# Kernel optimization log

Measured on AMD Instinct MI355X. Metric: run time of the kernel, lower is better.

## Reference

```python
import jax, jax.numpy as jnp
import numpy as np

D_MODEL = 1024
EPS_DT = 1e-4
LN_EPS = 1e-5


def _layernorm(y, gamma, beta):
    mu = jnp.mean(y, axis=-1, keepdims=True)
    var = jnp.var(y, axis=-1, keepdims=True)
    return (y - mu) * jax.lax.rsqrt(var + LN_EPS) * gamma + beta


def setup_inputs() -> dict:
    key = jax.random.key(0)
    ks = jax.random.split(key, 8)
    B, T, D = 8, 4096, D_MODEL
    s = 1.0 / np.sqrt(D)  # ~ torch Linear default init scale
    return {
        "x": jax.random.normal(ks[0], (B, T, D), jnp.float32),
        "delta_t": jax.random.uniform(ks[1], (B, T, D), jnp.float32),
        "log_decay": jnp.zeros((D,), jnp.float32),
        "W_in": jax.random.uniform(ks[2], (D, D), jnp.float32, -s, s),
        "b_in": jax.random.uniform(ks[3], (D,), jnp.float32, -s, s),
        "W_gate": jax.random.uniform(ks[4], (D, D), jnp.float32, -s, s),
        "b_gate": jax.random.uniform(ks[5], (D,), jnp.float32, -s, s),
        "W_out": jax.random.uniform(ks[6], (D, D), jnp.float32, -s, s),
        "b_out": jax.random.uniform(ks[7], (D,), jnp.float32, -s, s),
        "gamma": jnp.ones((D,), jnp.float32),
        "beta": jnp.zeros((D,), jnp.float32),
    }


def reference(x, delta_t, log_decay, W_in, b_in, W_gate, b_gate, W_out, b_out, gamma, beta):
    B, T, D = x.shape
    decay = jax.nn.softplus(log_decay) + 1e-4          # [D]
    dt = jnp.maximum(delta_t, EPS_DT)                   # [B,T,D]
    lamb = jnp.exp(-decay * dt)                         # [B,T,D]
    # Drive terms depend only on x -> precompute in parallel (big GEMMs).
    update = jnp.einsum('btd,ed->bte', x, W_in) + b_in
    gate = jax.nn.sigmoid(jnp.einsum('btd,ed->bte', x, W_gate) + b_gate)
    drive = (1.0 - lamb) * gate * update                # [B,T,D]

    def step(state, inputs):
        l_t, d_t = inputs
        state = l_t * state + d_t
        return state, state

    state0 = jnp.zeros((B, D), x.dtype)
    final_state, states = jax.lax.scan(
        step, state0,
        (jnp.swapaxes(lamb, 0, 1), jnp.swapaxes(drive, 0, 1)))
    states = jnp.swapaxes(states, 0, 1)                 # [B,T,D]
    # dropout is identity in eval mode
    y = states + jnp.einsum('btd,ed->bte', states, W_out) + b_out
    out = _layernorm(y, gamma, beta)
    return out, final_state
```

## Files before the change

### kernel.cpp

```cpp
#include <hip/hip_runtime.h>
#include <hip/hip_bf16.h>

#define D_MODEL 1024
#define BATCH 8
#define SEQ 4096
#define MROWS (BATCH*SEQ)
#define NC 64
#define CL 64

typedef __attribute__((ext_vector_type(4))) float f32x4;
typedef __attribute__((ext_vector_type(8))) short s16x8;

__device__ __forceinline__ unsigned short f2bf(float f){
  union { float f; unsigned int u; } v; v.f = f;
  return (unsigned short)((v.u + 0x7fffu + ((v.u >> 16) & 1u)) >> 16);
}
__device__ __forceinline__ float bf2f(unsigned int bits){
  union { unsigned int u; float f; } v; v.u = bits << 16; return v.f;
}

__device__ __forceinline__ void gload16(const void* g, void* l){
  __builtin_amdgcn_global_load_lds(
      (const __attribute__((address_space(1))) unsigned int*)g,
      (__attribute__((address_space(3))) unsigned int*)l, 16, 0, 0);
}

__global__ __launch_bounds__(256)
void prep_x_kernel(const float* __restrict__ x, unsigned short* __restrict__ xb, int n4){
  int i = blockIdx.x*256 + threadIdx.x;
  int stride = gridDim.x*256;
  for (; i < n4; i += stride){
    float4 v = ((const float4*)x)[i];
    ushort4 o;
    o.x = f2bf(v.x); o.y = f2bf(v.y); o.z = f2bf(v.z); o.w = f2bf(v.w);
    ((ushort4*)xb)[i] = o;
  }
}

__global__ __launch_bounds__(256)
void prep_w_kernel(const float* __restrict__ Wi, const float* __restrict__ Wg,
                   const float* __restrict__ Wo, const float* __restrict__ ld,
                   unsigned short* __restrict__ Wib, unsigned short* __restrict__ Wgb,
                   unsigned short* __restrict__ Wob, float* __restrict__ decay){
  int i = blockIdx.x*256 + threadIdx.x;
  {
    float4 a = ((const float4*)Wi)[i]; ushort4 o;
    o.x=f2bf(a.x); o.y=f2bf(a.y); o.z=f2bf(a.z); o.w=f2bf(a.w); ((ushort4*)Wib)[i]=o;
    a = ((const float4*)Wg)[i];
    o.x=f2bf(a.x); o.y=f2bf(a.y); o.z=f2bf(a.z); o.w=f2bf(a.w); ((ushort4*)Wgb)[i]=o;
    a = ((const float4*)Wo)[i];
    o.x=f2bf(a.x); o.y=f2bf(a.y); o.z=f2bf(a.z); o.w=f2bf(a.w); ((ushort4*)Wob)[i]=o;
  }
  if (i < D_MODEL){
    float v = ld[i];
    float sp = fmaxf(v, 0.f) + log1pf(expf(-fabsf(v)));
    decay[i] = sp + 1e-4f;
  }
}

__global__ __launch_bounds__(256, 2)
void gemm_dual_kernel(const unsigned short* __restrict__ Xb,
                      const unsigned short* __restrict__ Wib,
                      const unsigned short* __restrict__ Wgb,
                      const float* __restrict__ b_in,
                      const float* __restrict__ b_gate,
                      const float* __restrict__ decay,
                      const float* __restrict__ delta,
                      unsigned int* __restrict__ pack)
{
  __shared__ unsigned short sA[128*64];
  __shared__ unsigned short sBi[128*64];
  __shared__ unsigned short sBg[128*64];
  const int tid  = threadIdx.x;
  const int lane = tid & 63;
  const int wave = tid >> 6;
  const int wr = wave >> 1, wc = wave & 1;
  const int brow = blockIdx.y * 128;
  const int bcol = blockIdx.x * 128;

  const f32x4 zero = {0.f,0.f,0.f,0.f};
  f32x4 accU[4][4], accG[4][4];
  #pragma unroll
  for (int a=0;a<4;a++)
    #pragma unroll
    for (int b=0;b<4;b++){ accU[a][b]=zero; accG[a][b]=zero; }

  for (int kt = 0; kt < D_MODEL/64; ++kt){
    __syncthreads();
    const size_t kbyte = (size_t)kt*128;
    #pragma unroll
    for (int i=0;i<4;i++){
      const int ob = i*256 + wave*64;
      const int o  = ob + lane;
      const int r  = o >> 3;
      const int cb = (o & 7) * 16;
      gload16((const char*)Xb  + (size_t)(brow + r)*(D_MODEL*2) + kbyte + cb, (char*)sA  + (size_t)ob*16);
      gload16((const char*)Wib + (size_t)(bcol + r)*(D_MODEL*2) + kbyte + cb, (char*)sBi + (size_t)ob*16);
      gload16((const char*)Wgb + (size_t)(bcol + r)*(D_MODEL*2) + kbyte + cb, (char*)sBg + (size_t)ob*16);
    }
    __syncthreads();
    #pragma unroll
    for (int ks=0; ks<2; ++ks){
      s16x8 af[4], bi[4], bg[4];
      #pragma unroll
      for (int mi=0; mi<4; mi++){
        int row = wr*64 + mi*16 + (lane & 15);
        int boff = row*128 + ks*64 + ((lane>>4)*16);
        af[mi] = *(const s16x8*)((const char*)sA + boff);
      }
      #pragma unroll
      for (int ni=0; ni<4; ni++){
        int n = wc*64 + ni*16 + (lane & 15);
        int boff = n*128 + ks*64 + ((lane>>4)*16);
        bi[ni] = *(const s16x8*)((const char*)sBi + boff);
        bg[ni] = *(const s16x8*)((const char*)sBg + boff);
      }
      #pragma unroll
      for (int mi=0; mi<4; mi++)
        #pragma unroll
        for (int ni=0; ni<4; ni++){
          accU[mi][ni] = __builtin_amdgcn_mfma_f32_16x16x32_bf16(af[mi], bi[ni], accU[mi][ni], 0,0,0);
          accG[mi][ni] = __builtin_amdgcn_mfma_f32_16x16x32_bf16(af[mi], bg[ni], accG[mi][ni], 0,0,0);
        }
    }
  }
  #pragma unroll
  for (int ni=0; ni<4; ni++){
    const int col = bcol + wc*64 + ni*16 + (lane & 15);
    const float vb = b_in[col], vg = b_gate[col], dc = decay[col];
    #pragma unroll
    for (int mi=0; mi<4; mi++){
      #pragma unroll
      for (int q=0; q<4; q++){
        const int row = brow + wr*64 + mi*16 + ((lane>>4)*4) + q;
        const size_t idx = (size_t)row*D_MODEL + col;
        float u = accU[mi][ni][q] + vb;
        float z = accG[mi][ni][q] + vg;
        float g = 1.f/(1.f + __expf(-z));
        float dt = fmaxf(delta[idx], 1e-4f);
        float lam = __expf(-dc*dt);
        float omla = 1.f - lam;
        float drv = omla * g * u;
        pack[idx] = ((unsigned int)f2bf(drv) << 16) | (unsigned int)f2bf(omla);
      }
    }
  }
}

__global__ __launch_bounds__(256)
void scan_passA(const unsigned int* __restrict__ pack, float* __restrict__ cA, float* __restrict__ cB){
  const int d0 = (blockIdx.x*256 + threadIdx.x)*2;
  const int c = blockIdx.y, b = blockIdx.z;
  size_t base = ((size_t)b*SEQ + (size_t)c*CL)*D_MODEL + d0;
  float A0=1.f, A1=1.f, s0=0.f, s1=0.f;
  #pragma unroll 8
  for (int t=0;t<CL;t++){
    uint2 p = *(const uint2*)(pack + base + (size_t)t*D_MODEL);
    float om0 = bf2f(p.x & 0xffffu), dr0 = bf2f(p.x >> 16);
    float om1 = bf2f(p.y & 0xffffu), dr1 = bf2f(p.y >> 16);
    float l0 = 1.f - om0, l1 = 1.f - om1;
    A0 *= l0; A1 *= l1;
    s0 = fmaf(l0, s0, dr0);
    s1 = fmaf(l1, s1, dr1);
  }
  const size_t ci = ((size_t)b*NC + c)*D_MODEL + d0;
  *(float2*)(cA+ci) = make_float2(A0,A1);
  *(float2*)(cB+ci) = make_float2(s0,s1);
}

__global__ __launch_bounds__(256)
void scan_passB(const float* __restrict__ cA, const float* __restrict__ cB,
                float* __restrict__ cS, float* __restrict__ fstate){
  const int d0 = (blockIdx.x*256 + threadIdx.x)*2;
  const int b = blockIdx.y;
  float s0=0.f, s1=0.f;
  for (int c=0;c<NC;c++){
    const size_t ci = ((size_t)b*NC + c)*D_MODEL + d0;
    *(float2*)(cS+ci) = make_float2(s0,s1);
    float2 a  = *(const float2*)(cA+ci);
    float2 bb = *(const float2*)(cB+ci);
    s0 = fmaf(a.x, s0, bb.x);
    s1 = fmaf(a.y, s1, bb.y);
  }
  *(float2*)(fstate + (size_t)b*D_MODEL + d0) = make_float2(s0,s1);
}

__global__ __launch_bounds__(256)
void scan_passC(const unsigned int* __restrict__ pack, const float* __restrict__ cS,
                unsigned short* __restrict__ statesb){
  const int d0 = (blockIdx.x*256 + threadIdx.x)*2;
  const int c = blockIdx.y, b = blockIdx.z;
  float2 sv = *(const float2*)(cS + ((size_t)b*NC + c)*D_MODEL + d0);
  float s0 = sv.x, s1 = sv.y;
  size_t base = ((size_t)b*SEQ + (size_t)c*CL)*D_MODEL + d0;
  #pragma unroll 8
  for (int t=0;t<CL;t++){
    uint2 p = *(const uint2*)(pack + base + (size_t)t*D_MODEL);
    float om0 = bf2f(p.x & 0xffffu), dr0 = bf2f(p.x >> 16);
    float om1 = bf2f(p.y & 0xffffu), dr1 = bf2f(p.y >> 16);
    s0 = fmaf(-om0, s0, s0) + dr0;
    s1 = fmaf(-om1, s1, s1) + dr1;
    unsigned int w = ((unsigned int)f2bf(s1) << 16) | (unsigned int)f2bf(s0);
    *(unsigned int*)(statesb + base + (size_t)t*D_MODEL) = w;
  }
}

__global__ __launch_bounds__(256, 2)
void gemm_out_kernel(const unsigned short* __restrict__ Sb,
                     const unsigned short* __restrict__ Wob,
                     const float* __restrict__ b_out,
                     float* __restrict__ y)
{
  __shared__ unsigned short sA[128*64];
  __shared__ unsigned short sB[128*64];
  const int tid  = threadIdx.x;
  const int lane = tid & 63;
  const int wave = tid >> 6;
  const int wr = wave >> 1, wc = wave & 1;
  const int brow = blockIdx.y * 128;
  const int bcol = blockIdx.x * 128;

  const f32x4 zero = {0.f,0.f,0.f,0.f};
  f32x4 acc[4][4];
  #pragma unroll
  for (int a=0;a<4;a++)
    #pragma unroll
    for (int b=0;b<4;b++) acc[a][b]=zero;

  for (int kt = 0; kt < D_MODEL/64; ++kt){
    __syncthreads();
    const size_t kbyte = (size_t)kt*128;
    #pragma unroll
    for (int i=0;i<4;i++){
      const int ob = i*256 + wave*64;
      const int o  = ob + lane;
      const int r  = o >> 3;
      const int cb = (o & 7) * 16;
      gload16((const char*)Sb  + (size_t)(brow + r)*(D_MODEL*2) + kbyte + cb, (char*)sA + (size_t)ob*16);
      gload16((const char*)Wob + (size_t)(bcol + r)*(D_MODEL*2) + kbyte + cb, (char*)sB + (size_t)ob*16);
    }
    __syncthreads();
    #pragma unroll
    for (int ks=0; ks<2; ++ks){
      s16x8 af[4], bf[4];
      #pragma unroll
      for (int mi=0; mi<4; mi++){
        int row = wr*64 + mi*16 + (lane & 15);
        int boff = row*128 + ks*64 + ((lane>>4)*16);
        af[mi] = *(const s16x8*)((const char*)sA + boff);
      }
      #pragma unroll
      for (int ni=0; ni<4; ni++){
        int n = wc*64 + ni*16 + (lane & 15);
        int boff = n*128 + ks*64 + ((lane>>4)*16);
        bf[ni] = *(const s16x8*)((const char*)sB + boff);
      }
      #pragma unroll
      for (int mi=0; mi<4; mi++)
        #pragma unroll
        for (int ni=0; ni<4; ni++)
          acc[mi][ni] = __builtin_amdgcn_mfma_f32_16x16x32_bf16(af[mi], bf[ni], acc[mi][ni], 0,0,0);
    }
  }
  #pragma unroll
  for (int ni=0; ni<4; ni++){
    const int col = bcol + wc*64 + ni*16 + (lane & 15);
    const float vb = b_out[col];
    #pragma unroll
    for (int mi=0; mi<4; mi++){
      #pragma unroll
      for (int q=0; q<4; q++){
        const int row = brow + wr*64 + mi*16 + ((lane>>4)*4) + q;
        const size_t idx = (size_t)row*D_MODEL + col;
        y[idx] = acc[mi][ni][q] + bf2f((unsigned int)Sb[idx]) + vb;
      }
    }
  }
}

__global__ __launch_bounds__(256)
void ln_kernel(const float* __restrict__ y, const float* __restrict__ gamma,
               const float* __restrict__ beta, float* __restrict__ out)
{
  const int row = blockIdx.x;
  const int tid = threadIdx.x;
  const float4* yr = (const float4*)(y + (size_t)row*D_MODEL);
  float4 v = yr[tid];
  float s = v.x+v.y+v.z+v.w;
  float q = v.x*v.x + v.y*v.y + v.z*v.z + v.w*v.w;
  #pragma unroll
  for (int off=32; off>0; off>>=1){ s += __shfl_xor(s, off); q += __shfl_xor(q, off); }
  __shared__ float rs[4], rq[4];
  const int wave = tid>>6, lane = tid&63;
  if (lane==0){ rs[wave]=s; rq[wave]=q; }
  __syncthreads();
  float ts = rs[0]+rs[1]+rs[2]+rs[3];
  float tq = rq[0]+rq[1]+rq[2]+rq[3];
  float mu  = ts * (1.f/D_MODEL);
  float var = tq * (1.f/D_MODEL) - mu*mu;
  float inv = rsqrtf(var + 1e-5f);
  float4 g = ((const float4*)gamma)[tid];
  float4 b = ((const float4*)beta)[tid];
  float4 o;
  o.x = (v.x-mu)*inv*g.x + b.x;
  o.y = (v.y-mu)*inv*g.y + b.y;
  o.z = (v.z-mu)*inv*g.z + b.z;
  o.w = (v.w-mu)*inv*g.w + b.w;
  ((float4*)(out + (size_t)row*D_MODEL))[tid] = o;
}

extern "C" void kernel_launch(void* const* d_in, const int* in_sizes, int n_in,
                              void* d_out, int out_size, void* d_ws, size_t ws_size,
                              hipStream_t stream) {
  const float* x         = (const float*)d_in[0];
  const float* delta     = (const float*)d_in[1];
  const float* log_decay = (const float*)d_in[2];
  const float* W_in      = (const float*)d_in[3];
  const float* b_in      = (const float*)d_in[4];
  const float* W_gate    = (const float*)d_in[5];
  const float* b_gate    = (const float*)d_in[6];
  const float* W_out     = (const float*)d_in[7];
  const float* b_out     = (const float*)d_in[8];
  const float* gamma     = (const float*)d_in[9];
  const float* beta      = (const float*)d_in[10];

  char* w = (char*)d_ws;
  unsigned short* xb   = (unsigned short*)(w);
  unsigned short* Wib  = (unsigned short*)(w + 67108864);
  unsigned short* Wgb  = (unsigned short*)(w + 69206016);
  unsigned short* Wob  = (unsigned short*)(w + 71303168);
  float*          decay= (float*)        (w + 73400320);
  float*          cA   = (float*)        (w + 73404416);
  float*          cB   = (float*)        (w + 75501568);
  float*          cS   = (float*)        (w + 77598720);
  unsigned int*   pack = (unsigned int*) (w + 79695872);
  float*          ybuf = (float*)pack;
  unsigned short* statesb = xb;

  float* out    = (float*)d_out;
  float* fstate = out + (size_t)MROWS*D_MODEL;

  hipLaunchKernelGGL(prep_x_kernel, dim3(8192), dim3(256), 0, stream, x, xb, MROWS*D_MODEL/4);
  hipLaunchKernelGGL(prep_w_kernel, dim3(1024), dim3(256), 0, stream,
                     W_in, W_gate, W_out, log_decay, Wib, Wgb, Wob, decay);
  hipLaunchKernelGGL(gemm_dual_kernel, dim3(8,256), dim3(256), 0, stream,
                     xb, Wib, Wgb, b_in, b_gate, decay, delta, pack);
  hipLaunchKernelGGL(scan_passA, dim3(2,NC,BATCH), dim3(256), 0, stream, pack, cA, cB);
  hipLaunchKernelGGL(scan_passB, dim3(2,BATCH), dim3(256), 0, stream, cA, cB, cS, fstate);
  hipLaunchKernelGGL(scan_passC, dim3(2,NC,BATCH), dim3(256), 0, stream, pack, cS, statesb);
  hipLaunchKernelGGL(gemm_out_kernel, dim3(8,256), dim3(256), 0, stream, statesb, Wob, b_out, ybuf);
  hipLaunchKernelGGL(ln_kernel, dim3(MROWS), dim3(256), 0, stream, ybuf, gamma, beta, out);
}
```

Measured before the change: 472.8 us.

## Swizzle LDS tiles, remap block order, move residual add into layernorm

Both GEMMs now XOR-swizzle the 16-byte chunks of each LDS row, which is meant to remove bank conflicts on the fragment reads. They also use a 1D grid with a block-index remap so that consecutive blocks share A rows across the eight column tiles, improving L2 reuse. The bf16 residual read, previously a strided scalar load in the gemm_out epilogue, moves into the layernorm kernel as a vectorized ushort4 load. gemm_out's launch bounds go from 2 to 3 blocks per SM, which risks register spills.

```diff
diff --git a/kernel.cpp b/kernel.cpp
--- a/kernel.cpp
+++ b/kernel.cpp
@@ -75,8 +75,10 @@
   const int lane = tid & 63;
   const int wave = tid >> 6;
   const int wr = wave >> 1, wc = wave & 1;
-  const int brow = blockIdx.y * 128;
-  const int bcol = blockIdx.x * 128;
+  const int bid = blockIdx.x;
+  const int swz = ((bid & 7) << 8) | (bid >> 3);
+  const int bcol = (swz & 7) * 128;
+  const int brow = (swz >> 3) * 128;
 
   const f32x4 zero = {0.f,0.f,0.f,0.f};
   f32x4 accU[4][4], accG[4][4];
@@ -93,7 +95,7 @@
       const int ob = i*256 + wave*64;
       const int o  = ob + lane;
       const int r  = o >> 3;
-      const int cb = (o & 7) * 16;
+      const int cb = ((o & 7) ^ (r & 7)) * 16;
       gload16((const char*)Xb  + (size_t)(brow + r)*(D_MODEL*2) + kbyte + cb, (char*)sA  + (size_t)ob*16);
       gload16((const char*)Wib + (size_t)(bcol + r)*(D_MODEL*2) + kbyte + cb, (char*)sBi + (size_t)ob*16);
       gload16((const char*)Wgb + (size_t)(bcol + r)*(D_MODEL*2) + kbyte + cb, (char*)sBg + (size_t)ob*16);
@@ -105,15 +107,15 @@
       #pragma unroll
       for (int mi=0; mi<4; mi++){
         int row = wr*64 + mi*16 + (lane & 15);
-        int boff = row*128 + ks*64 + ((lane>>4)*16);
-        af[mi] = *(const s16x8*)((const char*)sA + boff);
+        int chunk = (ks*4 + (lane>>4)) ^ (row & 7);
+        af[mi] = *(const s16x8*)((const char*)sA + row*128 + chunk*16);
       }
       #pragma unroll
       for (int ni=0; ni<4; ni++){
         int n = wc*64 + ni*16 + (lane & 15);
-        int boff = n*128 + ks*64 + ((lane>>4)*16);
-        bi[ni] = *(const s16x8*)((const char*)sBi + boff);
-        bg[ni] = *(const s16x8*)((const char*)sBg + boff);
+        int chunk = (ks*4 + (lane>>4)) ^ (n & 7);
+        bi[ni] = *(const s16x8*)((const char*)sBi + n*128 + chunk*16);
+        bg[ni] = *(const s16x8*)((const char*)sBg + n*128 + chunk*16);
       }
       #pragma unroll
       for (int mi=0; mi<4; mi++)
@@ -205,7 +207,7 @@
   }
 }
 
-__global__ __launch_bounds__(256, 2)
+__global__ __launch_bounds__(256, 3)
 void gemm_out_kernel(const unsigned short* __restrict__ Sb,
                      const unsigned short* __restrict__ Wob,
                      const float* __restrict__ b_out,
@@ -217,8 +219,10 @@
   const int lane = tid & 63;
   const int wave = tid >> 6;
   const int wr = wave >> 1, wc = wave & 1;
-  const int brow = blockIdx.y * 128;
-  const int bcol = blockIdx.x * 128;
+  const int bid = blockIdx.x;
+  const int swz = ((bid & 7) << 8) | (bid >> 3);
+  const int bcol = (swz & 7) * 128;
+  const int brow = (swz >> 3) * 128;
 
   const f32x4 zero = {0.f,0.f,0.f,0.f};
   f32x4 acc[4][4];
@@ -235,7 +239,7 @@
       const int ob = i*256 + wave*64;
       const int o  = ob + lane;
       const int r  = o >> 3;
-      const int cb = (o & 7) * 16;
+      const int cb = ((o & 7) ^ (r & 7)) * 16;
       gload16((const char*)Sb  + (size_t)(brow + r)*(D_MODEL*2) + kbyte + cb, (char*)sA + (size_t)ob*16);
       gload16((const char*)Wob + (size_t)(bcol + r)*(D_MODEL*2) + kbyte + cb, (char*)sB + (size_t)ob*16);
     }
@@ -246,14 +250,14 @@
       #pragma unroll
       for (int mi=0; mi<4; mi++){
         int row = wr*64 + mi*16 + (lane & 15);
-        int boff = row*128 + ks*64 + ((lane>>4)*16);
-        af[mi] = *(const s16x8*)((const char*)sA + boff);
+        int chunk = (ks*4 + (lane>>4)) ^ (row & 7);
+        af[mi] = *(const s16x8*)((const char*)sA + row*128 + chunk*16);
       }
       #pragma unroll
       for (int ni=0; ni<4; ni++){
         int n = wc*64 + ni*16 + (lane & 15);
-        int boff = n*128 + ks*64 + ((lane>>4)*16);
-        bf[ni] = *(const s16x8*)((const char*)sB + boff);
+        int chunk = (ks*4 + (lane>>4)) ^ (n & 7);
+        bf[ni] = *(const s16x8*)((const char*)sB + n*128 + chunk*16);
       }
       #pragma unroll
       for (int mi=0; mi<4; mi++)
@@ -272,20 +276,22 @@
       for (int q=0; q<4; q++){
         const int row = brow + wr*64 + mi*16 + ((lane>>4)*4) + q;
         const size_t idx = (size_t)row*D_MODEL + col;
-        y[idx] = acc[mi][ni][q] + bf2f((unsigned int)Sb[idx]) + vb;
-      }
-    }
-  }
-}
-
-__global__ __launch_bounds__(256)
-void ln_kernel(const float* __restrict__ y, const float* __restrict__ gamma,
-               const float* __restrict__ beta, float* __restrict__ out)
+        y[idx] = acc[mi][ni][q] + vb;
+      }
+    }
+  }
+}
+
+__global__ __launch_bounds__(256)
+void ln_kernel(const float* __restrict__ y, const unsigned short* __restrict__ statesb,
+               const float* __restrict__ gamma, const float* __restrict__ beta,
+               float* __restrict__ out)
 {
   const int row = blockIdx.x;
   const int tid = threadIdx.x;
-  const float4* yr = (const float4*)(y + (size_t)row*D_MODEL);
-  float4 v = yr[tid];
+  float4 v = ((const float4*)(y + (size_t)row*D_MODEL))[tid];
+  ushort4 sb = ((const ushort4*)(statesb + (size_t)row*D_MODEL))[tid];
+  v.x += bf2f(sb.x); v.y += bf2f(sb.y); v.z += bf2f(sb.z); v.w += bf2f(sb.w);
   float s = v.x+v.y+v.z+v.w;
   float q = v.x*v.x + v.y*v.y + v.z*v.z + v.w*v.w;
   #pragma unroll
@@ -343,11 +349,11 @@
   hipLaunchKernelGGL(prep_x_kernel, dim3(8192), dim3(256), 0, stream, x, xb, MROWS*D_MODEL/4);
   hipLaunchKernelGGL(prep_w_kernel, dim3(1024), dim3(256), 0, stream,
                      W_in, W_gate, W_out, log_decay, Wib, Wgb, Wob, decay);
-  hipLaunchKernelGGL(gemm_dual_kernel, dim3(8,256), dim3(256), 0, stream,
+  hipLaunchKernelGGL(gemm_dual_kernel, dim3(2048), dim3(256), 0, stream,
                      xb, Wib, Wgb, b_in, b_gate, decay, delta, pack);
   hipLaunchKernelGGL(scan_passA, dim3(2,NC,BATCH), dim3(256), 0, stream, pack, cA, cB);
   hipLaunchKernelGGL(scan_passB, dim3(2,BATCH), dim3(256), 0, stream, cA, cB, cS, fstate);
   hipLaunchKernelGGL(scan_passC, dim3(2,NC,BATCH), dim3(256), 0, stream, pack, cS, statesb);
-  hipLaunchKernelGGL(gemm_out_kernel, dim3(8,256), dim3(256), 0, stream, statesb, Wob, b_out, ybuf);
-  hipLaunchKernelGGL(ln_kernel, dim3(MROWS), dim3(256), 0, stream, ybuf, gamma, beta, out);
-}
+  hipLaunchKernelGGL(gemm_out_kernel, dim3(2048), dim3(256), 0, stream, statesb, Wob, b_out, ybuf);
+  hipLaunchKernelGGL(ln_kernel, dim3(MROWS), dim3(256), 0, stream, ybuf, statesb, gamma, beta, out);
+}
```

After: 425.0 us. 10.1% less time.
